# Optimization experiments

Hardware: AMD Instinct MI355X
Metric: run time of the kernel (lower is better)

Reference implementation:

```python
import jax, jax.numpy as jnp
import numpy as np

HEADS = 12
KEY_DIM = 16
B, C, H, W = 16, 384, 64, 64


def _hard_swish(x):
    return x * jnp.clip(x + 3.0, 0.0, 6.0) / 6.0


def _affine(x, g, b):
    # Inference-mode BatchNorm folded into per-channel scale/shift (NCHW).
    return x * g[:, None, None] + b[:, None, None]


def _pw(x, w):
    # 1x1 conv as a channel contraction: x [B,Cin,H,W], w [Cout,Cin].
    return jnp.einsum('bchw,oc->bohw', x, w)


def setup_inputs() -> dict:
    key = jax.random.key(0)
    ks = jax.random.split(key, 20)
    d = {}
    d['x'] = jax.random.normal(ks[0], (B, C, H, W), dtype=jnp.float32)
    d['rnd_offset'] = jax.random.uniform(ks[1], (B, 2, 1, 1), dtype=jnp.float32) * 6.0 - 3.0
    S = HEADS * KEY_DIM  # 192
    d['proj_w'] = jax.random.normal(ks[2], (3 * S, C + 2), dtype=jnp.float32) * 0.05
    d['proj_g'] = jax.random.uniform(ks[3], (3 * S,), dtype=jnp.float32) + 0.5
    d['proj_b'] = jax.random.normal(ks[4], (3 * S,), dtype=jnp.float32) * 0.1
    d['vp2_w'] = jax.random.normal(ks[5], (C, S), dtype=jnp.float32) * 0.05
    d['vp2_g'] = jax.random.uniform(ks[6], (C,), dtype=jnp.float32) + 0.5
    d['vp2_b'] = jax.random.normal(ks[7], (C,), dtype=jnp.float32) * 0.1
    d['dw_w'] = jax.random.normal(ks[8], (C, 1, 5, 5), dtype=jnp.float32) * 0.1
    d['dw_g'] = jax.random.uniform(ks[9], (C,), dtype=jnp.float32) + 0.5
    d['dw_b'] = jax.random.normal(ks[10], (C,), dtype=jnp.float32) * 0.1
    d['pw1_w'] = jax.random.normal(ks[11], (4 * C, C), dtype=jnp.float32) * 0.05
    d['pw1_g'] = jax.random.uniform(ks[12], (4 * C,), dtype=jnp.float32) + 0.5
    d['pw1_b'] = jax.random.normal(ks[13], (4 * C,), dtype=jnp.float32) * 0.1
    d['pw2_w'] = jax.random.normal(ks[14], (C, 4 * C), dtype=jnp.float32) * 0.05
    d['out_g'] = jax.random.uniform(ks[15], (C,), dtype=jnp.float32) + 0.5
    d['out_b'] = jax.random.normal(ks[16], (C,), dtype=jnp.float32) * 0.1
    d['rz_attn'] = jnp.float32(0.1)
    d['rz_ffn'] = jnp.float32(0.1)
    d['embed_strength'] = jnp.float32(-10.0)
    return d


def reference(x, rnd_offset, proj_w, proj_g, proj_b, vp2_w, vp2_g, vp2_b,
              dw_w, dw_g, dw_b, pw1_w, pw1_g, pw1_b, pw2_w, out_g, out_b,
              rz_attn, rz_ffn, embed_strength):
    b, c, h, w = x.shape
    # --- learned-strength positional embedding with random per-image offset ---
    xp = jnp.arange(w, dtype=x.dtype) / 1000.0
    yp = jnp.arange(h, dtype=x.dtype) / 1000.0
    xx, yy = jnp.meshgrid(xp, yp, indexing='xy')      # each (H, W)
    pos = jnp.stack([xx, yy], axis=0)[None]           # (1, 2, H, W)
    pos = jnp.exp(embed_strength) * (pos + rnd_offset)  # (B, 2, H, W)
    x_emb = jnp.concatenate([x, pos], axis=1)         # (B, C+2, H, W)

    # --- qkv projection (1x1 conv + BN + ReLU), computed in fp32 ---
    proj = jax.nn.relu(_affine(_pw(x_emb, proj_w), proj_g, proj_b))
    proj = proj.astype(jnp.float32)

    S = HEADS * KEY_DIM
    N = h * w

    def get_slice(i):
        # (B, S, H, W) slice -> (B*heads, N, key_dim)
        s = proj[:, i * S:(i + 1) * S]
        return s.reshape(b * HEADS, KEY_DIM, N).transpose(0, 2, 1)

    q, k, v = get_slice(0), get_slice(1), get_slice(2)

    # --- non-causal linear attention: Q (K^T V) / (Q sum(K)) ---
    ktv = jnp.einsum('bnd,bne->bde', k, v)            # (B*heads, d, d)
    numer = jnp.einsum('bnd,bde->bne', q, ktv)        # (B*heads, N, d)
    denom = jnp.einsum('bnd,bd->bn', q, k.sum(axis=1))[..., None]  # (B*heads, N, 1)
    out = numer / jnp.maximum(denom, 1e-4)
    out = out.transpose(0, 2, 1).reshape(b, S, h, w)  # (B, heads*key_dim, H, W)

    # --- value projection back to channels ---
    out = jax.nn.relu(_affine(_pw(out, vp2_w), vp2_g, vp2_b))
    y = x + rz_attn * out

    # --- FFN: depthwise 5x5 -> expand 1x1 -> project 1x1 (+ BNs) ---
    z = jax.lax.conv_general_dilated(
        y, dw_w, window_strides=(1, 1), padding='SAME',
        dimension_numbers=('NCHW', 'OIHW', 'NCHW'), feature_group_count=c)
    z = _hard_swish(_affine(z, dw_g, dw_b))
    z = _hard_swish(_affine(_pw(z, pw1_w), pw1_g, pw1_b))
    z = _affine(_pw(z, pw2_w), out_g, out_b)
    return y + rz_ffn * z
```

## Files before the change

### kernel.cpp

```cpp
#include <hip/hip_runtime.h>
#include <cstdint>

typedef unsigned short u16;
typedef __attribute__((ext_vector_type(8))) __bf16 bf16x8;
typedef __attribute__((ext_vector_type(4))) float f32x4;

__device__ __forceinline__ u16 f2bf(float f) {
    union { float f; uint32_t u; } v; v.f = f;
    uint32_t u = v.u;
    uint32_t r = (u + 0x7fffu + ((u >> 16) & 1u)) >> 16;
    return (u16)r;
}
__device__ __forceinline__ float bf2f(u16 h) {
    union { uint32_t u; float f; } v; v.u = ((uint32_t)h) << 16;
    return v.f;
}

__device__ __forceinline__ void ld_lds16(const u16* g, u16* l) {
    __builtin_amdgcn_global_load_lds(
        (const __attribute__((address_space(1))) uint32_t*)g,
        (__attribute__((address_space(3))) uint32_t*)l, 16, 0, 0);
}

__global__ __launch_bounds__(256) void prep(
    const float* __restrict__ proj_w, const float* __restrict__ proj_g,
    const float* __restrict__ proj_b, const float* __restrict__ vp2_w,
    const float* __restrict__ pw1_w, const float* __restrict__ pw2_w,
    const float* __restrict__ dw_w,
    u16* __restrict__ w1p, u16* __restrict__ w2, u16* __restrict__ w3,
    u16* __restrict__ w4, float* __restrict__ gp, float2* __restrict__ dwp)
{
    int i = blockIdx.x * 256 + threadIdx.x;
    if (i < 245760) {
        int o = i / 384, k = i - o * 384;
        w1p[i] = (o < 576) ? f2bf(proj_w[o * 386 + k]) : (u16)0;
        return;
    }
    i -= 245760;
    if (i < 73728) { w2[i] = f2bf(vp2_w[i]); return; }
    i -= 73728;
    if (i < 589824) { w3[i] = f2bf(pw1_w[i]); return; }
    i -= 589824;
    if (i < 589824) { w4[i] = f2bf(pw2_w[i]); return; }
    i -= 589824;
    if (i < 2560) {
        int which = i / 640, o = i - which * 640;
        float v = 0.f;
        if (o < 576) {
            v = (which == 0) ? proj_g[o] : (which == 1) ? proj_b[o]
                : (which == 2) ? proj_w[o * 386 + 384] : proj_w[o * 386 + 385];
        }
        gp[i] = v; return;
    }
    i -= 2560;
    if (i < 4800) {
        int tap = i / 192, cp = i - tap * 192;
        dwp[i] = make_float2(dw_w[(2 * cp) * 25 + tap], dw_w[(2 * cp + 1) * 25 + tap]);
    }
}

__global__ __launch_bounds__(256) void transpose_x(const float* __restrict__ x,
                                                   u16* __restrict__ xt)
{
    __shared__ float tile[64][65];
    int b = blockIdx.x, n0 = blockIdx.y * 64, c0 = blockIdx.z * 64;
    int t = threadIdx.x;
    int jj = t & 63, i0 = t >> 6;
    #pragma unroll
    for (int r = 0; r < 16; r++) {
        int ci = r * 4 + i0;
        tile[ci][jj] = x[((size_t)b * 384 + c0 + ci) * 4096 + n0 + jj];
    }
    __syncthreads();
    #pragma unroll
    for (int r = 0; r < 16; r++) {
        int ni = r * 4 + i0;
        xt[(size_t)(b * 4096 + n0 + ni) * 384 + c0 + jj] = f2bf(tile[jj][ni]);
    }
}

__global__ __launch_bounds__(256) void transpose_out(const u16* __restrict__ zf,
                                                     float* __restrict__ out)
{
    __shared__ float tile[64][65];
    int b = blockIdx.x, n0 = blockIdx.y * 64, c0 = blockIdx.z * 64;
    int t = threadIdx.x;
    int jj = t & 63, i0 = t >> 6;
    #pragma unroll
    for (int r = 0; r < 16; r++) {
        int ni = r * 4 + i0;
        tile[ni][jj] = bf2f(zf[(size_t)(b * 4096 + n0 + ni) * 384 + c0 + jj]);
    }
    __syncthreads();
    #pragma unroll
    for (int r = 0; r < 16; r++) {
        int ci = r * 4 + i0;
        out[((size_t)b * 384 + c0 + ci) * 4096 + n0 + jj] = tile[jj][ci];
    }
}

template <int MODE, int IM, int JN>
__global__ __launch_bounds__(256) void gemm_nhwc(
    const u16* __restrict__ A, const u16* __restrict__ W,
    u16* __restrict__ out, int K, int Osz, int nOT,
    const float* __restrict__ g, const float* __restrict__ bb,
    const float* __restrict__ w1x, const float* __restrict__ w1y,
    const u16* __restrict__ res, const float* __restrict__ sc,
    const float* __restrict__ rnd)
{
    constexpr int BK = 32;
    constexpr int BM = IM * 32;
    constexpr int BN = JN * 32;
    constexpr int GA = IM / 2;
    constexpr int GB = JN / 2;
    constexpr int NCH = GA + GB;
    constexpr int NBUF = ((BM + BN) * 64 * 3 <= 49152) ? 3 : 2;
    __shared__ u16 smem[NBUF * (BM + BN) * BK];

    const int tid = threadIdx.x;
    const int lane = tid & 63;
    const int wv = tid >> 6;
    const int wm = (wv >> 1) * (IM * 16);
    const int wn = (wv & 1) * (JN * 16);

    const int nwg = gridDim.x;
    const int q8 = nwg >> 3;
    const int b1 = (blockIdx.x & 7) * q8 + (blockIdx.x >> 3);
    const int mt = b1 / nOT;
    const int ot = b1 - mt * nOT;
    const int m0 = mt * BM;
    const int o0 = ot * BN;

    const int q = lane >> 4;
    const int mr = lane & 15;
    const int ks = (q ^ ((mr >> 1) & 3)) * 8;

    const int tq = tid >> 2;
    const int sl = tid & 3;
    const int tk = (sl ^ ((tq >> 1) & 3)) * 8;

    size_t ga[GA], gb[GB];
    int la[GA], lb[GB];
    #pragma unroll
    for (int gi = 0; gi < GA; gi++) {
        ga[gi] = (size_t)(m0 + gi * 64 + tq) * K + tk;
        la[gi] = (gi * 64 + tq) * BK + sl * 8;
    }
    #pragma unroll
    for (int gi = 0; gi < GB; gi++) {
        gb[gi] = (size_t)(o0 + gi * 64 + tq) * K + tk;
        lb[gi] = (gi * 64 + tq) * BK + sl * 8;
    }

#define STAGE(TILE, BUFI)                                                    \
    {                                                                        \
        const size_t ko = (size_t)(TILE) * BK;                               \
        u16* sAb = smem + (BUFI) * (BM * BK);                                \
        u16* sBb = smem + NBUF * (BM * BK) + (BUFI) * (BN * BK);             \
        _Pragma("unroll")                                                    \
        for (int gi = 0; gi < GA; gi++)                                      \
            ld_lds16(A + ga[gi] + ko, sAb + la[gi]);                         \
        _Pragma("unroll")                                                    \
        for (int gi = 0; gi < GB; gi++)                                      \
            ld_lds16(W + gb[gi] + ko, sBb + lb[gi]);                         \
    }

    f32x4 acc[IM][JN] = {};
    const int nIter = K >> 5;

    STAGE(0, 0)
    if (NBUF == 3 && nIter > 1) STAGE(1, 1)

    int buf = 0;
    for (int t = 0; t < nIter; ++t) {
        if constexpr (NBUF == 3) {
            if (t + 1 < nIter)
                asm volatile("s_waitcnt vmcnt(%0)" ::"i"(NCH) : "memory");
            else
                asm volatile("s_waitcnt vmcnt(0)" ::: "memory");
        } else {
            asm volatile("s_waitcnt vmcnt(0)" ::: "memory");
        }
        __builtin_amdgcn_s_barrier();
        __builtin_amdgcn_sched_barrier(0);
        if (t + NBUF - 1 < nIter) {
            int nb = buf + (NBUF - 1); if (nb >= NBUF) nb -= NBUF;
            STAGE(t + NBUF - 1, nb)
        }
        const u16* sAr = smem + buf * (BM * BK);
        const u16* sBr = smem + NBUF * (BM * BK) + buf * (BN * BK);
        bf16x8 af[IM], bfr[JN];
        #pragma unroll
        for (int i = 0; i < IM; i++)
            af[i] = *(const bf16x8*)&sAr[(wm + i * 16 + mr) * BK + ks];
        #pragma unroll
        for (int j = 0; j < JN; j++)
            bfr[j] = *(const bf16x8*)&sBr[(wn + j * 16 + mr) * BK + ks];
        __builtin_amdgcn_s_setprio(1);
        #pragma unroll
        for (int i = 0; i < IM; i++)
            #pragma unroll
            for (int j = 0; j < JN; j++)
                acc[i][j] = __builtin_amdgcn_mfma_f32_16x16x32_bf16(af[i], bfr[j], acc[i][j], 0, 0, 0);
        __builtin_amdgcn_s_setprio(0);
        buf++; if (buf == NBUF) buf = 0;
    }
#undef STAGE

    float* st = (float*)smem;
    constexpr int P = BM / 32;
    constexpr int HP = IM / 2;
    constexpr int NG = BN / 128;
    const int row_l = tid >> 3;
    const int cs16 = (tid & 7) * 16;

    float E = 0.f, offx = 0.f, offy = 0.f, rz = 0.f;
    if constexpr (MODE == 1) {
        E = expf(sc[0]);
        int bimg = m0 >> 12;
        offx = rnd[bimg * 2 + 0];
        offy = rnd[bimg * 2 + 1];
    }
    if constexpr (MODE == 2 || MODE == 4) rz = sc[0];

    float gv[NG][16], bv[NG][16];
    #pragma unroll
    for (int gg = 0; gg < NG; gg++)
        #pragma unroll
        for (int c = 0; c < 4; c++) {
            *(float4*)&gv[gg][c * 4] = *(const float4*)(g + o0 + gg * 128 + cs16 + c * 4);
            *(float4*)&bv[gg][c * 4] = *(const float4*)(bb + o0 + gg * 128 + cs16 + c * 4);
        }
    float wxv[16], wyv[16];
    if constexpr (MODE == 1) {
        #pragma unroll
        for (int c = 0; c < 4; c++) {
            *(float4*)&wxv[c * 4] = *(const float4*)(w1x + o0 + cs16 + c * 4);
            *(float4*)&wyv[c * 4] = *(const float4*)(w1y + o0 + cs16 + c * 4);
        }
    }

    #pragma unroll
    for (int p = 0; p < P; ++p) {
        __syncthreads();
        if ((wv >> 1) == p / HP) {
            const int ib = (p % HP) * 2;
            #pragma unroll
            for (int ii = 0; ii < 2; ++ii)
                #pragma unroll
                for (int j = 0; j < JN; ++j)
                    #pragma unroll
                    for (int r = 0; r < 4; ++r)
                        st[(ii * 16 + q * 4 + r) * (BN + 2) + wn + j * 16 + mr] =
                            acc[ib + ii][j][r];
        }
        __syncthreads();
        const int pix = m0 + p * 32 + row_l;
        float px = 0.f, py = 0.f;
        if constexpr (MODE == 1) {
            int n = pix & 4095;
            px = E * ((float)(n & 63) * 0.001f + offx);
            py = E * ((float)(n >> 6) * 0.001f + offy);
        }
        #pragma unroll
        for (int gg = 0; gg < NG; ++gg) {
            const int ob = o0 + gg * 128 + cs16;
            float vals[16];
            #pragma unroll
            for (int e = 0; e < 16; ++e)
                vals[e] = st[row_l * (BN + 2) + gg * 128 + cs16 + e];
            u16 rv[16];
            if constexpr (MODE == 2 || MODE == 4) {
                #pragma unroll
                for (int c = 0; c < 2; c++)
                    *(float4*)&rv[c * 8] = *(const float4*)(res + (size_t)pix * 384 + ob + c * 8);
            }
            u16 ov[16];
            #pragma unroll
            for (int e = 0; e < 16; ++e) {
                float v = vals[e];
                if constexpr (MODE == 1) {
                    v += px * wxv[e] + py * wyv[e];
                    v = fmaxf(gv[gg][e] * v + bv[gg][e], 0.f);
                } else if constexpr (MODE == 2) {
                    v = fmaxf(gv[gg][e] * v + bv[gg][e], 0.f);
                    v = bf2f(rv[e]) + rz * v;
                } else if constexpr (MODE == 3) {
                    float tv = gv[gg][e] * v + bv[gg][e];
                    v = tv * fminf(fmaxf(tv + 3.f, 0.f), 6.f) * (1.f / 6.f);
                } else {
                    float tv = gv[gg][e] * v + bv[gg][e];
                    v = bf2f(rv[e]) + rz * tv;
                }
                ov[e] = f2bf(v);
            }
            #pragma unroll
            for (int c = 0; c < 2; c++)
                *(float4*)(out + (size_t)pix * Osz + ob + c * 8) = *(const float4*)&ov[c * 8];
        }
    }
}

__global__ __launch_bounds__(256) void attn_ktv(const u16* __restrict__ proj,
                                                float* __restrict__ ktvp)
{
    int bh = blockIdx.x;
    int ch = blockIdx.y;
    int b = bh / 12, h = bh - b * 12;
    const u16* base = proj + (size_t)b * 4096 * 640;
    int kc = 192 + h * 16, vc = 384 + h * 16;
    __shared__ u16 ks[256 * 16];
    __shared__ u16 vs[256 * 16];
    int t = threadIdx.x;
    int d = t >> 4, e = t & 15;
    float acc = 0.f, ksum = 0.f;
    for (int n0 = ch * 1024; n0 < ch * 1024 + 1024; n0 += 256) {
        __syncthreads();
        const u16* r = base + (size_t)(n0 + t) * 640;
        ((float4*)&ks[t * 16])[0] = ((const float4*)(r + kc))[0];
        ((float4*)&ks[t * 16])[1] = ((const float4*)(r + kc))[1];
        ((float4*)&vs[t * 16])[0] = ((const float4*)(r + vc))[0];
        ((float4*)&vs[t * 16])[1] = ((const float4*)(r + vc))[1];
        __syncthreads();
        #pragma unroll 8
        for (int n = 0; n < 256; n++)
            acc += bf2f(ks[n * 16 + d]) * bf2f(vs[n * 16 + e]);
        if (t < 16) {
            #pragma unroll 8
            for (int n = 0; n < 256; n++) ksum += bf2f(ks[n * 16 + t]);
        }
    }
    float* o = ktvp + ((size_t)bh * 4 + ch) * 272;
    o[t] = acc;
    if (t < 16) o[256 + t] = ksum;
}

__global__ __launch_bounds__(256) void attn_apply(const u16* __restrict__ proj,
                                                  const float* __restrict__ ktvp,
                                                  u16* __restrict__ att)
{
    int bh = blockIdx.x;
    int b = bh / 12, h = bh - b * 12;
    __shared__ float kt[272];
    int t = threadIdx.x;
    {
        const float* p = ktvp + (size_t)bh * 4 * 272;
        kt[t] = p[t] + p[272 + t] + p[544 + t] + p[816 + t];
        if (t < 16) {
            int u = 256 + t;
            kt[u] = p[u] + p[272 + u] + p[544 + u] + p[816 + u];
        }
    }
    __syncthreads();
    int n = blockIdx.y * 256 + t;
    const u16* qr = proj + (size_t)(b * 4096 + n) * 640 + h * 16;
    float qv[16];
    #pragma unroll
    for (int d = 0; d < 16; d++) qv[d] = bf2f(qr[d]);
    float denom = 0.f;
    #pragma unroll
    for (int d = 0; d < 16; d++) denom += qv[d] * kt[256 + d];
    float rcp = 1.f / fmaxf(denom, 1e-4f);
    u16* op = att + (size_t)(b * 4096 + n) * 192 + h * 16;
    #pragma unroll
    for (int e = 0; e < 16; e++) {
        float s = 0.f;
        #pragma unroll
        for (int d = 0; d < 16; d++) s += qv[d] * kt[d * 16 + e];
        op[e] = f2bf(s * rcp);
    }
}

__global__ __launch_bounds__(192) void dwconv(const u16* __restrict__ y,
                                              const float2* __restrict__ wt,
                                              const float* __restrict__ g,
                                              const float* __restrict__ bc,
                                              u16* __restrict__ z)
{
    const int cp = threadIdx.x;
    const int xc = blockIdx.x;
    const int b  = blockIdx.y;
    const int c0 = cp * 2;

    float2 wv[25];
    #pragma unroll
    for (int t = 0; t < 25; t++) wv[t] = wt[t * 192 + cp];
    const float g0 = g[c0], g1 = g[c0 + 1];
    const float b0 = bc[c0], b1 = bc[c0 + 1];

    const size_t ibase = (size_t)b * 4096;
    const u16* ycol = y + ibase * 384 + c0;

    uint32_t r0[5], r1[5], r2[5], r3[5], r4[5];

#define LOADROW(yy, dst)                                                     \
    {                                                                        \
        if ((unsigned)(yy) < 64u) {                                          \
            const u16* rp = ycol + (size_t)(yy) * 64 * 384;                  \
            _Pragma("unroll")                                                \
            for (int dx = 0; dx < 5; dx++) {                                 \
                int xx = xc + dx - 2;                                        \
                dst[dx] = ((unsigned)xx < 64u)                               \
                              ? *(const uint32_t*)(rp + (size_t)xx * 384)    \
                              : 0u;                                          \
            }                                                                \
        } else {                                                             \
            _Pragma("unroll")                                                \
            for (int dx = 0; dx < 5; dx++) dst[dx] = 0u;                     \
        }                                                                    \
    }

#define COMPUTE(yr, A, B, C, D, E)                                           \
    if ((yr) < 64) {                                                         \
        float a0 = 0.f, a1 = 0.f;                                            \
        _Pragma("unroll")                                                    \
        for (int dx = 0; dx < 5; dx++) {                                     \
            uint32_t p;                                                      \
            p = A[dx];                                                       \
            a0 += wv[dx].x * bf2f((u16)(p & 0xffffu));                       \
            a1 += wv[dx].y * bf2f((u16)(p >> 16));                           \
            p = B[dx];                                                       \
            a0 += wv[5 + dx].x * bf2f((u16)(p & 0xffffu));                   \
            a1 += wv[5 + dx].y * bf2f((u16)(p >> 16));                       \
            p = C[dx];                                                       \
            a0 += wv[10 + dx].x * bf2f((u16)(p & 0xffffu));                  \
            a1 += wv[10 + dx].y * bf2f((u16)(p >> 16));                      \
            p = D[dx];                                                       \
            a0 += wv[15 + dx].x * bf2f((u16)(p & 0xffffu));                  \
            a1 += wv[15 + dx].y * bf2f((u16)(p >> 16));                      \
            p = E[dx];                                                       \
            a0 += wv[20 + dx].x * bf2f((u16)(p & 0xffffu));                  \
            a1 += wv[20 + dx].y * bf2f((u16)(p >> 16));                      \
        }                                                                    \
        float t0 = g0 * a0 + b0;                                             \
        float t1 = g1 * a1 + b1;                                             \
        t0 = t0 * fminf(fmaxf(t0 + 3.f, 0.f), 6.f) * (1.f / 6.f);            \
        t1 = t1 * fminf(fmaxf(t1 + 3.f, 0.f), 6.f) * (1.f / 6.f);            \
        uint32_t packed = (uint32_t)f2bf(t0) | ((uint32_t)f2bf(t1) << 16);   \
        *(uint32_t*)(z + (ibase + (size_t)(yr) * 64 + xc) * 384 + c0) = packed; \
    }

#define STEP(yr, A, B, C, D, E)                                              \
    COMPUTE(yr, A, B, C, D, E)                                               \
    LOADROW((yr) + 3, A)

    LOADROW(-2, r0)
    LOADROW(-1, r1)
    LOADROW(0, r2)
    LOADROW(1, r3)
    LOADROW(2, r4)

    for (int base = 0; base < 65; base += 5) {
        STEP(base + 0, r0, r1, r2, r3, r4)
        STEP(base + 1, r1, r2, r3, r4, r0)
        STEP(base + 2, r2, r3, r4, r0, r1)
        STEP(base + 3, r3, r4, r0, r1, r2)
        STEP(base + 4, r4, r0, r1, r2, r3)
    }
#undef STEP
#undef COMPUTE
#undef LOADROW
}

extern "C" void kernel_launch(void* const* d_in, const int* in_sizes, int n_in,
                              void* d_out, int out_size, void* d_ws, size_t ws_size,
                              hipStream_t stream)
{
    (void)in_sizes; (void)n_in; (void)out_size; (void)ws_size;
    const float* x       = (const float*)d_in[0];
    const float* rnd     = (const float*)d_in[1];
    const float* proj_w  = (const float*)d_in[2];
    const float* proj_g  = (const float*)d_in[3];
    const float* proj_b  = (const float*)d_in[4];
    const float* vp2_w   = (const float*)d_in[5];
    const float* vp2_g   = (const float*)d_in[6];
    const float* vp2_b   = (const float*)d_in[7];
    const float* dw_w    = (const float*)d_in[8];
    const float* dw_g    = (const float*)d_in[9];
    const float* dw_b    = (const float*)d_in[10];
    const float* pw1_w   = (const float*)d_in[11];
    const float* pw1_g   = (const float*)d_in[12];
    const float* pw1_b   = (const float*)d_in[13];
    const float* pw2_w   = (const float*)d_in[14];
    const float* out_g   = (const float*)d_in[15];
    const float* out_b   = (const float*)d_in[16];
    const float* rz_attn = (const float*)d_in[17];
    const float* rz_ffn  = (const float*)d_in[18];
    const float* es      = (const float*)d_in[19];
    float* out = (float*)d_out;

    char* ws = (char*)d_ws;
    u16*   xt   = (u16*)(ws + 0);
    u16*   att  = (u16*)(ws + 50331648);
    u16*   z2   = (u16*)(ws + 0);
    u16*   proj = (u16*)(ws + 201326592);
    u16*   z1   = proj;
    u16*   z4   = proj;
    u16*   yt   = (u16*)(ws + 285212672);
    u16*   w1p  = (u16*)(ws + 335753216);
    u16*   w2   = (u16*)(ws + 336244736);
    u16*   w3   = (u16*)(ws + 336392192);
    u16*   w4   = (u16*)(ws + 337571840);
    float* gp   = (float*)(ws + 338751488);
    float2* dwp = (float2*)(ws + 338761728);
    float* ktvp = (float*)(ws + 338800128);

    prep<<<5885, 256, 0, stream>>>(proj_w, proj_g, proj_b, vp2_w, pw1_w, pw2_w,
                                   dw_w, w1p, w2, w3, w4, gp, dwp);
    transpose_x<<<dim3(16, 64, 6), 256, 0, stream>>>(x, xt);
    gemm_nhwc<1, 4, 4><<<2560, 256, 0, stream>>>(xt, w1p, proj, 384, 640, 5,
        gp, gp + 640, gp + 1280, gp + 1920, nullptr, es, rnd);
    attn_ktv<<<dim3(192, 4), 256, 0, stream>>>(proj, ktvp);
    attn_apply<<<dim3(192, 16), 256, 0, stream>>>(proj, ktvp, att);
    gemm_nhwc<2, 8, 4><<<768, 256, 0, stream>>>(att, w2, yt, 192, 384, 3,
        vp2_g, vp2_b, nullptr, nullptr, xt, rz_attn, nullptr);
    dwconv<<<dim3(64, 16), 192, 0, stream>>>(yt, dwp, dw_g, dw_b, z1);
    gemm_nhwc<3, 4, 8><<<3072, 256, 0, stream>>>(z1, w3, z2, 384, 1536, 6,
        pw1_g, pw1_b, nullptr, nullptr, nullptr, nullptr, nullptr);
    gemm_nhwc<4, 8, 4><<<768, 256, 0, stream>>>(z2, w4, z4, 1536, 384, 3,
        out_g, out_b, nullptr, nullptr, yt, rz_ffn, nullptr);
    transpose_out<<<dim3(16, 64, 6), 256, 0, stream>>>(z4, out);
}
```

Baseline: 699.8 us.

## Split GEMM K-tile loads into two half-stage phases for non-4x4 tiles

For GEMM tile shapes other than 4x4, the main loop becomes double-buffered with each K-tile's loads split into two phases. The first half of the fragments is computed while the first half of the next tile's loads are in flight, then the second half follows after a second wait and barrier. The intent is finer-grained overlap of global-to-LDS traffic with MFMA work and less LDS use, at the cost of an extra barrier per iteration. The epilogue staging stride is also padded to BN+4 so accumulators can be read back as aligned 16-byte vector loads.

```diff
diff --git a/kernel.cpp b/kernel.cpp
--- a/kernel.cpp
+++ b/kernel.cpp
@@ -113,9 +113,12 @@
     constexpr int BN = JN * 32;
     constexpr int GA = IM / 2;
     constexpr int GB = JN / 2;
-    constexpr int NCH = GA + GB;
-    constexpr int NBUF = ((BM + BN) * 64 * 3 <= 49152) ? 3 : 2;
-    __shared__ u16 smem[NBUF * (BM + BN) * BK];
+    constexpr bool LEGACY = (IM == 4 && JN == 4);
+    constexpr bool SPB = (JN >= IM);
+    constexpr int NBUF = LEGACY ? 3 : 2;
+    constexpr int NP1 = LEGACY ? 0 : (SPB ? GB / 2 : GA / 2);
+    constexpr int NP0 = LEGACY ? 0 : (GA + GB - NP1);
+    __shared__ __align__(16) u16 smem[NBUF * (BM + BN) * BK];
 
     const int tid = threadIdx.x;
     const int lane = tid & 63;
@@ -152,62 +155,156 @@
         lb[gi] = (gi * 64 + tq) * BK + sl * 8;
     }
 
-#define STAGE(TILE, BUFI)                                                    \
-    {                                                                        \
-        const size_t ko = (size_t)(TILE) * BK;                               \
-        u16* sAb = smem + (BUFI) * (BM * BK);                                \
-        u16* sBb = smem + NBUF * (BM * BK) + (BUFI) * (BN * BK);             \
-        _Pragma("unroll")                                                    \
-        for (int gi = 0; gi < GA; gi++)                                      \
-            ld_lds16(A + ga[gi] + ko, sAb + la[gi]);                         \
-        _Pragma("unroll")                                                    \
-        for (int gi = 0; gi < GB; gi++)                                      \
-            ld_lds16(W + gb[gi] + ko, sBb + lb[gi]);                         \
-    }
+    auto stage_all = [&](int tile, int bufi) {
+        const size_t ko = (size_t)tile * BK;
+        u16* sAb = smem + bufi * (BM * BK);
+        u16* sBb = smem + NBUF * (BM * BK) + bufi * (BN * BK);
+        #pragma unroll
+        for (int gi = 0; gi < GA; gi++) ld_lds16(A + ga[gi] + ko, sAb + la[gi]);
+        #pragma unroll
+        for (int gi = 0; gi < GB; gi++) ld_lds16(W + gb[gi] + ko, sBb + lb[gi]);
+    };
+    auto stage_s0 = [&](int tile, int bufi) {
+        const size_t ko = (size_t)tile * BK;
+        u16* sAb = smem + bufi * (BM * BK);
+        u16* sBb = smem + NBUF * (BM * BK) + bufi * (BN * BK);
+        if constexpr (SPB) {
+            #pragma unroll
+            for (int gi = 0; gi < GA; gi++) ld_lds16(A + ga[gi] + ko, sAb + la[gi]);
+            #pragma unroll
+            for (int gi = 0; gi < GB; gi += 2) ld_lds16(W + gb[gi] + ko, sBb + lb[gi]);
+        } else {
+            #pragma unroll
+            for (int gi = 0; gi < GA; gi += 2) ld_lds16(A + ga[gi] + ko, sAb + la[gi]);
+            #pragma unroll
+            for (int gi = 0; gi < GB; gi++) ld_lds16(W + gb[gi] + ko, sBb + lb[gi]);
+        }
+    };
+    auto stage_s1 = [&](int tile, int bufi) {
+        const size_t ko = (size_t)tile * BK;
+        u16* sAb = smem + bufi * (BM * BK);
+        u16* sBb = smem + NBUF * (BM * BK) + bufi * (BN * BK);
+        if constexpr (SPB) {
+            #pragma unroll
+            for (int gi = 1; gi < GB; gi += 2) ld_lds16(W + gb[gi] + ko, sBb + lb[gi]);
+        } else {
+            #pragma unroll
+            for (int gi = 1; gi < GA; gi += 2) ld_lds16(A + ga[gi] + ko, sAb + la[gi]);
+        }
+    };
 
     f32x4 acc[IM][JN] = {};
     const int nIter = K >> 5;
-
-    STAGE(0, 0)
-    if (NBUF == 3 && nIter > 1) STAGE(1, 1)
-
     int buf = 0;
-    for (int t = 0; t < nIter; ++t) {
-        if constexpr (NBUF == 3) {
+
+    if constexpr (LEGACY) {
+        stage_all(0, 0);
+        if (nIter > 1) stage_all(1, 1);
+        for (int t = 0; t < nIter; ++t) {
+            if (t + 1 < nIter) asm volatile("s_waitcnt vmcnt(4)" ::: "memory");
+            else               asm volatile("s_waitcnt vmcnt(0)" ::: "memory");
+            __builtin_amdgcn_s_barrier();
+            __builtin_amdgcn_sched_barrier(0);
+            if (t + 2 < nIter) {
+                int nb = buf + 2; if (nb >= 3) nb -= 3;
+                stage_all(t + 2, nb);
+            }
+            const u16* sAr = smem + buf * (BM * BK);
+            const u16* sBr = smem + NBUF * (BM * BK) + buf * (BN * BK);
+            bf16x8 af[IM], bfr[JN];
+            #pragma unroll
+            for (int i = 0; i < IM; i++)
+                af[i] = *(const bf16x8*)&sAr[(wm + i * 16 + mr) * BK + ks];
+            #pragma unroll
+            for (int j = 0; j < JN; j++)
+                bfr[j] = *(const bf16x8*)&sBr[(wn + j * 16 + mr) * BK + ks];
+            __builtin_amdgcn_s_setprio(1);
+            #pragma unroll
+            for (int i = 0; i < IM; i++)
+                #pragma unroll
+                for (int j = 0; j < JN; j++)
+                    acc[i][j] = __builtin_amdgcn_mfma_f32_16x16x32_bf16(af[i], bfr[j], acc[i][j], 0, 0, 0);
+            __builtin_amdgcn_s_setprio(0);
+            buf++; if (buf == 3) buf = 0;
+        }
+    } else {
+        stage_s0(0, 0);
+        stage_s1(0, 0);
+        for (int t = 0; t < nIter; ++t) {
+            const u16* sAr = smem + buf * (BM * BK);
+            const u16* sBr = smem + NBUF * (BM * BK) + buf * (BN * BK);
+            bf16x8 af[IM], bfr[JN];
+            asm volatile("s_waitcnt vmcnt(%0)" ::"i"(NP1) : "memory");
+            __builtin_amdgcn_s_barrier();
+            __builtin_amdgcn_sched_barrier(0);
+            if constexpr (SPB) {
+                #pragma unroll
+                for (int i = 0; i < IM; i++)
+                    af[i] = *(const bf16x8*)&sAr[(wm + i * 16 + mr) * BK + ks];
+                #pragma unroll
+                for (int j = 0; j < JN / 2; j++)
+                    bfr[j] = *(const bf16x8*)&sBr[(wn + j * 16 + mr) * BK + ks];
+            } else {
+                #pragma unroll
+                for (int i = 0; i < IM / 2; i++)
+                    af[i] = *(const bf16x8*)&sAr[(wm + i * 16 + mr) * BK + ks];
+                #pragma unroll
+                for (int j = 0; j < JN; j++)
+                    bfr[j] = *(const bf16x8*)&sBr[(wn + j * 16 + mr) * BK + ks];
+            }
+            if (t + 1 < nIter) stage_s0(t + 1, buf ^ 1);
+            __builtin_amdgcn_s_setprio(1);
+            if constexpr (SPB) {
+                #pragma unroll
+                for (int i = 0; i < IM; i++)
+                    #pragma unroll
+                    for (int j = 0; j < JN / 2; j++)
+                        acc[i][j] = __builtin_amdgcn_mfma_f32_16x16x32_bf16(af[i], bfr[j], acc[i][j], 0, 0, 0);
+            } else {
+                #pragma unroll
+                for (int i = 0; i < IM / 2; i++)
+                    #pragma unroll
+                    for (int j = 0; j < JN; j++)
+                        acc[i][j] = __builtin_amdgcn_mfma_f32_16x16x32_bf16(af[i], bfr[j], acc[i][j], 0, 0, 0);
+            }
+            __builtin_amdgcn_s_setprio(0);
             if (t + 1 < nIter)
-                asm volatile("s_waitcnt vmcnt(%0)" ::"i"(NCH) : "memory");
+                asm volatile("s_waitcnt vmcnt(%0)" ::"i"(NP0) : "memory");
             else
                 asm volatile("s_waitcnt vmcnt(0)" ::: "memory");
-        } else {
-            asm volatile("s_waitcnt vmcnt(0)" ::: "memory");
-        }
-        __builtin_amdgcn_s_barrier();
-        __builtin_amdgcn_sched_barrier(0);
-        if (t + NBUF - 1 < nIter) {
-            int nb = buf + (NBUF - 1); if (nb >= NBUF) nb -= NBUF;
-            STAGE(t + NBUF - 1, nb)
-        }
-        const u16* sAr = smem + buf * (BM * BK);
-        const u16* sBr = smem + NBUF * (BM * BK) + buf * (BN * BK);
-        bf16x8 af[IM], bfr[JN];
-        #pragma unroll
-        for (int i = 0; i < IM; i++)
-            af[i] = *(const bf16x8*)&sAr[(wm + i * 16 + mr) * BK + ks];
-        #pragma unroll
-        for (int j = 0; j < JN; j++)
-            bfr[j] = *(const bf16x8*)&sBr[(wn + j * 16 + mr) * BK + ks];
-        __builtin_amdgcn_s_setprio(1);
-        #pragma unroll
-        for (int i = 0; i < IM; i++)
-            #pragma unroll
-            for (int j = 0; j < JN; j++)
-                acc[i][j] = __builtin_amdgcn_mfma_f32_16x16x32_bf16(af[i], bfr[j], acc[i][j], 0, 0, 0);
-        __builtin_amdgcn_s_setprio(0);
-        buf++; if (buf == NBUF) buf = 0;
-    }
-#undef STAGE
+            __builtin_amdgcn_s_barrier();
+            __builtin_amdgcn_sched_barrier(0);
+            if constexpr (SPB) {
+                #pragma unroll
+                for (int j = JN / 2; j < JN; j++)
+                    bfr[j] = *(const bf16x8*)&sBr[(wn + j * 16 + mr) * BK + ks];
+            } else {
+                #pragma unroll
+                for (int i = IM / 2; i < IM; i++)
+                    af[i] = *(const bf16x8*)&sAr[(wm + i * 16 + mr) * BK + ks];
+            }
+            if (t + 1 < nIter) stage_s1(t + 1, buf ^ 1);
+            __builtin_amdgcn_s_setprio(1);
+            if constexpr (SPB) {
+                #pragma unroll
+                for (int i = 0; i < IM; i++)
+                    #pragma unroll
+                    for (int j = JN / 2; j < JN; j++)
+                        acc[i][j] = __builtin_amdgcn_mfma_f32_16x16x32_bf16(af[i], bfr[j], acc[i][j], 0, 0, 0);
+            } else {
+                #pragma unroll
+                for (int i = IM / 2; i < IM; i++)
+                    #pragma unroll
+                    for (int j = 0; j < JN; j++)
+                        acc[i][j] = __builtin_amdgcn_mfma_f32_16x16x32_bf16(af[i], bfr[j], acc[i][j], 0, 0, 0);
+            }
+            __builtin_amdgcn_s_setprio(0);
+            buf ^= 1;
+        }
+    }
 
     float* st = (float*)smem;
+    constexpr int LDE = BN + 4;
     constexpr int P = BM / 32;
     constexpr int HP = IM / 2;
     constexpr int NG = BN / 128;
@@ -251,7 +348,7 @@
                 for (int j = 0; j < JN; ++j)
                     #pragma unroll
                     for (int r = 0; r < 4; ++r)
-                        st[(ii * 16 + q * 4 + r) * (BN + 2) + wn + j * 16 + mr] =
+                        st[(ii * 16 + q * 4 + r) * LDE + wn + j * 16 + mr] =
                             acc[ib + ii][j][r];
         }
         __syncthreads();
@@ -267,8 +364,9 @@
             const int ob = o0 + gg * 128 + cs16;
             float vals[16];
             #pragma unroll
-            for (int e = 0; e < 16; ++e)
-                vals[e] = st[row_l * (BN + 2) + gg * 128 + cs16 + e];
+            for (int c = 0; c < 4; ++c)
+                *(f32x4*)&vals[c * 4] =
+                    *(const f32x4*)&st[row_l * LDE + gg * 128 + cs16 + c * 4];
             u16 rv[16];
             if constexpr (MODE == 2 || MODE == 4) {
                 #pragma unroll
```

Result: no change. 692.5 us (-1.0%).
